# Optimization experiments

Hardware: AMD Instinct MI355X
Metric: run time of the kernel (lower is better)

## Reference

```python
import jax, jax.numpy as jnp
import numpy as np

EDGE_THRESHOLD = 0.1
N_NODES, IN_DIM, OUT_DIM, EDGE_DIM = 512, 128, 128, 64
LN_EPS = 1e-5


def setup_inputs() -> dict:
    key = jax.random.key(0)
    ks = jax.random.split(key, 20)
    s = 0.05
    d_in2e = 2 * IN_DIM + EDGE_DIM
    return {
        "node_features": jax.random.normal(ks[0], (N_NODES, IN_DIM), jnp.float32),
        "W": jax.random.normal(ks[1], (N_NODES, N_NODES), jnp.float32),
        "M": jax.random.normal(ks[2], (N_NODES, N_NODES), jnp.float32),
        "edge_features": jax.random.normal(ks[3], (N_NODES, N_NODES, EDGE_DIM), jnp.float32),
        # node_mlp: Linear(in,out) -> ReLU -> Linear(out,out)
        "node_w1": jax.random.normal(ks[4], (IN_DIM, OUT_DIM), jnp.float32) * s,
        "node_b1": jnp.zeros((OUT_DIM,), jnp.float32),
        "node_w2": jax.random.normal(ks[5], (OUT_DIM, OUT_DIM), jnp.float32) * s,
        "node_b2": jnp.zeros((OUT_DIM,), jnp.float32),
        # directed_msg: Linear(2*in+edge_dim,out) -> ReLU -> Linear(out,out)
        "dir_w1": jax.random.normal(ks[6], (d_in2e, OUT_DIM), jnp.float32) * s,
        "dir_b1": jnp.zeros((OUT_DIM,), jnp.float32),
        "dir_w2": jax.random.normal(ks[7], (OUT_DIM, OUT_DIM), jnp.float32) * s,
        "dir_b2": jnp.zeros((OUT_DIM,), jnp.float32),
        # bidirected_msg: Linear(2*in,out) -> ReLU -> Linear(out,out)
        "bi_w1": jax.random.normal(ks[8], (2 * IN_DIM, OUT_DIM), jnp.float32) * s,
        "bi_b1": jnp.zeros((OUT_DIM,), jnp.float32),
        "bi_w2": jax.random.normal(ks[9], (OUT_DIM, OUT_DIM), jnp.float32) * s,
        "bi_b2": jnp.zeros((OUT_DIM,), jnp.float32),
        # LayerNorm(out)
        "ln_g": jnp.ones((OUT_DIM,), jnp.float32),
        "ln_b": jnp.zeros((OUT_DIM,), jnp.float32),
    }


def reference(node_features, W, M, edge_features,
              node_w1, node_b1, node_w2, node_b2,
              dir_w1, dir_b1, dir_w2, dir_b2,
              bi_w1, bi_b1, bi_w2, bi_b2,
              ln_g, ln_b):
    n, d = node_features.shape
    x = node_features

    # self path
    h_self = jax.nn.relu(x @ node_w1 + node_b1) @ node_w2 + node_b2

    # directed messages: msg[j,i] = MLP([x_j, x_i, e_{j,i}]), weight = |W[j,i]| masked.
    # First linear split by concat blocks to avoid materializing (n,n,2d+e).
    src = x @ dir_w1[:d]                 # (n,h)   parent/source term
    tgt = x @ dir_w1[d:2 * d]            # (n,h)   target term
    edg = jnp.einsum('jie,eh->jih', edge_features, dir_w1[2 * d:])  # (n,n,h)
    h1 = jax.nn.relu(src[:, None, :] + tgt[None, :, :] + edg + dir_b1)  # (n,n,h) [j,i]
    msg_d = h1 @ dir_w2 + dir_b2         # (n,n,out)
    absW = jnp.abs(W)
    wd = jnp.where(absW > EDGE_THRESHOLD, absW, 0.0)  # (n,n) [parent j, target i]
    h_dir = jnp.einsum('jio,ji->io', msg_d, wd)

    # bidirected messages: for node i, neighbors j: MLP([x_j, x_i]), weight = |M[i,j]| masked, j != i
    bsrc = x @ bi_w1[:d]
    btgt = x @ bi_w1[d:]
    h1b = jax.nn.relu(bsrc[:, None, :] + btgt[None, :, :] + bi_b1)  # (n,n,h) [j,i]
    msg_b = h1b @ bi_w2 + bi_b2
    absM = jnp.abs(M)
    wb = jnp.where(absM > EDGE_THRESHOLD, absM, 0.0)
    wb = wb * (1.0 - jnp.eye(n, dtype=wb.dtype))  # exclude self
    h_bi = jnp.einsum('jio,ij->io', msg_b, wb)

    h = h_self + h_dir + h_bi
    mu = jnp.mean(h, axis=-1, keepdims=True)
    var = jnp.mean(jnp.square(h - mu), axis=-1, keepdims=True)
    return (h - mu) * jax.lax.rsqrt(var + LN_EPS) * ln_g + ln_b
```

## Files before the change

### kernel.cpp

```cpp
#include <hip/hip_runtime.h>
#include <hip/hip_bf16.h>
#include <cstdint>

#define NN 512
#define DD 128
#define EE 64
#define THR 0.1f
#define NCHUNK 16

typedef __bf16 bf16x8 __attribute__((ext_vector_type(8)));
typedef float  f32x4  __attribute__((ext_vector_type(4)));

__global__ __launch_bounds__(256) void k_zero(float* __restrict__ p, int n)
{
    int i = blockIdx.x * 256 + threadIdx.x;
    if (i < n) p[i] = 0.f;
}

__global__ __launch_bounds__(128) void k_pre(
    const float* __restrict__ x,
    const float* __restrict__ dw1, const float* __restrict__ bw1,
    const float* __restrict__ nw1, const float* __restrict__ nb1,
    float* __restrict__ src, float* __restrict__ tgt,
    float* __restrict__ bsrc, float* __restrict__ btgt, float* __restrict__ hmid)
{
    const int i0 = blockIdx.x * 4;
    const int h  = threadIdx.x;
    const int which = blockIdx.y;
    const float* B; float* outp;
    switch (which) {
        case 0:  B = dw1;          outp = src;  break;
        case 1:  B = dw1 + DD*DD;  outp = tgt;  break;
        case 2:  B = bw1;          outp = bsrc; break;
        case 3:  B = bw1 + DD*DD;  outp = btgt; break;
        default: B = nw1;          outp = hmid; break;
    }
    __shared__ float sx[4][DD];
    for (int idx = h; idx < 4*DD; idx += DD)
        sx[idx >> 7][idx & 127] = x[i0*DD + idx];
    __syncthreads();
    float a0=0.f, a1=0.f, a2=0.f, a3=0.f;
    for (int k = 0; k < DD; ++k) {
        float w = B[k*DD + h];
        a0 = fmaf(sx[0][k], w, a0);
        a1 = fmaf(sx[1][k], w, a1);
        a2 = fmaf(sx[2][k], w, a2);
        a3 = fmaf(sx[3][k], w, a3);
    }
    if (which == 4) {
        float bb = nb1[h];
        a0 = fmaxf(a0+bb, 0.f); a1 = fmaxf(a1+bb, 0.f);
        a2 = fmaxf(a2+bb, 0.f); a3 = fmaxf(a3+bb, 0.f);
    }
    outp[(i0+0)*DD + h] = a0;
    outp[(i0+1)*DD + h] = a1;
    outp[(i0+2)*DD + h] = a2;
    outp[(i0+3)*DD + h] = a3;
}

__global__ __launch_bounds__(256, 2) void k_dir(
    const float* __restrict__ ef, const float* __restrict__ W,
    const float* __restrict__ dw1, const float* __restrict__ db1,
    const float* __restrict__ src, const float* __restrict__ tgt,
    float* __restrict__ td_base, float* __restrict__ wsum_d, int partial)
{
    const int i0    = blockIdx.x * 16;
    const int jbase = blockIdx.y * 32;
    const int tid   = threadIdx.x;
    const int wave  = tid >> 6, lane = tid & 63;
    const int lrow  = lane & 15, lhi = lane >> 4;

    __shared__ float s_src[32][DD];
    __shared__ float s_wd[32][16];
    __shared__ float s_acc[4][16][DD];

    for (int idx = tid; idx < 32*DD; idx += 256)
        s_src[idx >> 7][idx & 127] = src[jbase*DD + idx];
    for (int idx = tid; idx < 32*16; idx += 256) {
        int jj = idx >> 4, il = idx & 15;
        float w = fabsf(W[(size_t)(jbase + jj)*NN + i0 + il]);
        s_wd[jj][il] = (w > THR) ? w : 0.0f;
    }

    bf16x8 bfrag[8][2];
    #pragma unroll
    for (int nf = 0; nf < 8; ++nf)
        #pragma unroll
        for (int kf = 0; kf < 2; ++kf) {
            bf16x8 t;
            #pragma unroll
            for (int e = 0; e < 8; ++e)
                t[e] = (__bf16)dw1[(2*DD + kf*32 + lhi*8 + e)*DD + nf*16 + lrow];
            bfrag[nf][kf] = t;
        }

    float tpre[8][4];
    #pragma unroll
    for (int nf = 0; nf < 8; ++nf)
        #pragma unroll
        for (int r = 0; r < 4; ++r) {
            int hh = nf*16 + lrow;
            tpre[nf][r] = tgt[(i0 + lhi*4 + r)*DD + hh] + db1[hh];
        }

    float acc[8][4] = {};
    __syncthreads();

    const float* ebase = ef + ((size_t)(jbase + wave)*NN + i0)*EE + lrow*EE + lhi*8;
    const size_t jstep = (size_t)4 * NN * EE;
    float4 a0 = *(const float4*)(ebase + 0);
    float4 a1 = *(const float4*)(ebase + 4);
    float4 a2 = *(const float4*)(ebase + 32);
    float4 a3 = *(const float4*)(ebase + 36);

    #pragma unroll 2
    for (int it = 0; it < 8; ++it) {
        float4 c0 = a0, c1 = a1, c2 = a2, c3 = a3;
        if (it < 7) {
            const float* np = ebase + (size_t)(it + 1)*jstep;
            a0 = *(const float4*)(np + 0);
            a1 = *(const float4*)(np + 4);
            a2 = *(const float4*)(np + 32);
            a3 = *(const float4*)(np + 36);
        }
        const int jj = wave + it*4;

        bf16x8 af0, af1;
        af0[0]=(__bf16)c0.x; af0[1]=(__bf16)c0.y; af0[2]=(__bf16)c0.z; af0[3]=(__bf16)c0.w;
        af0[4]=(__bf16)c1.x; af0[5]=(__bf16)c1.y; af0[6]=(__bf16)c1.z; af0[7]=(__bf16)c1.w;
        af1[0]=(__bf16)c2.x; af1[1]=(__bf16)c2.y; af1[2]=(__bf16)c2.z; af1[3]=(__bf16)c2.w;
        af1[4]=(__bf16)c3.x; af1[5]=(__bf16)c3.y; af1[6]=(__bf16)c3.z; af1[7]=(__bf16)c3.w;

        float wdv[4];
        #pragma unroll
        for (int r = 0; r < 4; ++r) wdv[r] = s_wd[jj][lhi*4 + r];

        #pragma unroll
        for (int nf = 0; nf < 8; ++nf) {
            f32x4 z = {0.f, 0.f, 0.f, 0.f};
            z = __builtin_amdgcn_mfma_f32_16x16x32_bf16(af0, bfrag[nf][0], z, 0, 0, 0);
            z = __builtin_amdgcn_mfma_f32_16x16x32_bf16(af1, bfrag[nf][1], z, 0, 0, 0);
            float sv = s_src[jj][nf*16 + lrow];
            #pragma unroll
            for (int r = 0; r < 4; ++r) {
                float v = z[r] + sv + tpre[nf][r];
                acc[nf][r] = fmaf(wdv[r], fmaxf(v, 0.f), acc[nf][r]);
            }
        }
    }

    #pragma unroll
    for (int nf = 0; nf < 8; ++nf)
        #pragma unroll
        for (int r = 0; r < 4; ++r)
            s_acc[wave][lhi*4 + r][nf*16 + lrow] = acc[nf][r];
    __syncthreads();

    float* dst = td_base + (partial ? (size_t)blockIdx.y * (NN*DD) : 0);
    for (int idx = tid; idx < 16*DD; idx += 256) {
        int il = idx >> 7, hh = idx & 127;
        float s = s_acc[0][il][hh] + s_acc[1][il][hh] + s_acc[2][il][hh] + s_acc[3][il][hh];
        int o = (i0 + il)*DD + hh;
        if (partial) dst[o] = s; else atomicAdd(&dst[o], s);
    }
    if (tid < 16) {
        float s = 0.f;
        #pragma unroll
        for (int jj = 0; jj < 32; ++jj) s += s_wd[jj][tid];
        if (partial) wsum_d[blockIdx.y * NN + i0 + tid] = s;
        else         atomicAdd(&wsum_d[i0 + tid], s);
    }
}

__global__ __launch_bounds__(256) void k_bidir(
    const float* __restrict__ M, const float* __restrict__ bsrc,
    const float* __restrict__ btgt, const float* __restrict__ bb1,
    float* __restrict__ tb_base, float* __restrict__ wsum_b, int partial)
{
    const int i0    = blockIdx.x * 16;
    const int jbase = blockIdx.y * 32;
    const int tid   = threadIdx.x;
    const int il    = tid >> 4;
    const int hg    = tid & 15;

    __shared__ float s_wb[16][32];
    __shared__ float s_bs[32][DD];

    for (int idx = tid; idx < 16*32; idx += 256) {
        int r = idx >> 5, jj = idx & 31;
        float m = fabsf(M[(size_t)(i0 + r)*NN + jbase + jj]);
        float w = (m > THR) ? m : 0.f;
        if (i0 + r == jbase + jj) w = 0.f;
        s_wb[r][jj] = w;
    }
    for (int idx = tid; idx < 32*DD; idx += 256)
        s_bs[idx >> 7][idx & 127] = bsrc[jbase*DD + idx];
    __syncthreads();

    float bt[8], acc[8] = {};
    #pragma unroll
    for (int r = 0; r < 8; ++r) {
        int hh = hg*8 + r;
        bt[r] = btgt[(i0 + il)*DD + hh] + bb1[hh];
    }
    for (int jj = 0; jj < 32; ++jj) {
        float w = s_wb[il][jj];
        const float* sp = &s_bs[jj][hg*8];
        float4 v0 = *(const float4*)sp;
        float4 v1 = *(const float4*)(sp + 4);
        acc[0] = fmaf(w, fmaxf(v0.x + bt[0], 0.f), acc[0]);
        acc[1] = fmaf(w, fmaxf(v0.y + bt[1], 0.f), acc[1]);
        acc[2] = fmaf(w, fmaxf(v0.z + bt[2], 0.f), acc[2]);
        acc[3] = fmaf(w, fmaxf(v0.w + bt[3], 0.f), acc[3]);
        acc[4] = fmaf(w, fmaxf(v1.x + bt[4], 0.f), acc[4]);
        acc[5] = fmaf(w, fmaxf(v1.y + bt[5], 0.f), acc[5]);
        acc[6] = fmaf(w, fmaxf(v1.z + bt[6], 0.f), acc[6]);
        acc[7] = fmaf(w, fmaxf(v1.w + bt[7], 0.f), acc[7]);
    }
    float* dst = tb_base + (partial ? (size_t)blockIdx.y * (NN*DD) : 0);
    #pragma unroll
    for (int r = 0; r < 8; ++r) {
        int o = (i0 + il)*DD + hg*8 + r;
        if (partial) dst[o] = acc[r]; else atomicAdd(&dst[o], acc[r]);
    }
    if (tid < 16) {
        float s = 0.f;
        #pragma unroll
        for (int jj = 0; jj < 32; ++jj) s += s_wb[tid][jj];
        if (partial) wsum_b[blockIdx.y * NN + i0 + tid] = s;
        else         atomicAdd(&wsum_b[i0 + tid], s);
    }
}

__global__ __launch_bounds__(256) void k_final(
    const float* __restrict__ hmid, const float* __restrict__ nw2, const float* __restrict__ nb2,
    const float* __restrict__ td,   const float* __restrict__ dw2, const float* __restrict__ db2,
    const float* __restrict__ wsd,
    const float* __restrict__ tb,   const float* __restrict__ bw2, const float* __restrict__ bb2,
    const float* __restrict__ wsb,
    const float* __restrict__ lng,  const float* __restrict__ lnb,
    float* __restrict__ out, int cd, int cb, int wpart)
{
    const int tid = threadIdx.x;
    const int r   = tid >> 7;
    const int h   = tid & 127;
    const int row = blockIdx.x * 2 + r;
    const int o   = row * DD + h;

    __shared__ float sm[2][DD], sd[2][DD], sb[2][DD];
    __shared__ float red[4];

    float vm = hmid[o];
    float s1 = 0.f, s2 = 0.f;
    #pragma unroll 4
    for (int c = 0; c < cd; ++c) s1 += td[(size_t)c*(NN*DD) + o];
    #pragma unroll 4
    for (int c = 0; c < cb; ++c) s2 += tb[(size_t)c*(NN*DD) + o];
    sm[r][h] = vm; sd[r][h] = s1; sb[r][h] = s2;
    __syncthreads();

    float wsum_d_row, wsum_b_row;
    if (wpart) {
        float a = 0.f, b = 0.f;
        #pragma unroll
        for (int c = 0; c < NCHUNK; ++c) {
            a += wsd[c*NN + row];
            b += wsb[c*NN + row];
        }
        wsum_d_row = a; wsum_b_row = b;
    } else {
        wsum_d_row = wsd[row]; wsum_b_row = wsb[row];
    }

    float acc = nb2[h] + wsum_d_row*db2[h] + wsum_b_row*bb2[h];
    #pragma unroll 4
    for (int k = 0; k < DD; ++k) {
        acc += sm[r][k]*nw2[k*DD + h] + sd[r][k]*dw2[k*DD + h] + sb[r][k]*bw2[k*DD + h];
    }

    const int wid = tid >> 6;
    float s = acc;
    #pragma unroll
    for (int off = 32; off > 0; off >>= 1) s += __shfl_down(s, off);
    if ((tid & 63) == 0) red[wid] = s;
    __syncthreads();
    float mu = (red[2*r] + red[2*r + 1]) * (1.0f/128.0f);
    float dv = acc - mu;
    float q  = dv * dv;
    __syncthreads();
    #pragma unroll
    for (int off = 32; off > 0; off >>= 1) q += __shfl_down(q, off);
    if ((tid & 63) == 0) red[wid] = q;
    __syncthreads();
    float var = (red[2*r] + red[2*r + 1]) * (1.0f/128.0f);
    out[o] = dv * rsqrtf(var + 1e-5f) * lng[h] + lnb[h];
}

extern "C" void kernel_launch(void* const* d_in, const int* in_sizes, int n_in,
                              void* d_out, int out_size, void* d_ws, size_t ws_size,
                              hipStream_t stream)
{
    (void)in_sizes; (void)n_in; (void)out_size;
    const float* x   = (const float*)d_in[0];
    const float* W   = (const float*)d_in[1];
    const float* M   = (const float*)d_in[2];
    const float* ef  = (const float*)d_in[3];
    const float* nw1 = (const float*)d_in[4];
    const float* nb1 = (const float*)d_in[5];
    const float* nw2 = (const float*)d_in[6];
    const float* nb2 = (const float*)d_in[7];
    const float* dw1 = (const float*)d_in[8];
    const float* db1 = (const float*)d_in[9];
    const float* dw2 = (const float*)d_in[10];
    const float* db2 = (const float*)d_in[11];
    const float* bw1 = (const float*)d_in[12];
    const float* bb1 = (const float*)d_in[13];
    const float* bw2 = (const float*)d_in[14];
    const float* bb2 = (const float*)d_in[15];
    const float* lng = (const float*)d_in[16];
    const float* lnb = (const float*)d_in[17];
    float* out = (float*)d_out;
    float* ws  = (float*)d_ws;

    const size_t TD = (size_t)NN * DD;
    const size_t WS_PART = (size_t)NCHUNK * NN;
    const size_t PART_FLOATS = 32*TD + 2*WS_PART + 5*TD;
    const int partial = (ws_size >= PART_FLOATS * 4) ? 1 : 0;

    float *t_dir, *t_bi, *wsd, *wsb, *base;
    if (partial) {
        t_dir = ws;
        t_bi  = ws + 16*TD;
        wsd   = ws + 32*TD;
        wsb   = wsd + WS_PART;
        base  = wsb + WS_PART;
    } else {
        t_dir = ws;
        t_bi  = ws + TD;
        wsd   = ws + 2*TD;
        wsb   = wsd + 512;
        base  = ws + 2*TD + 1024;
        int nz = (int)(2*TD + 1024);
        k_zero<<<(nz + 255)/256, 256, 0, stream>>>(ws, nz);
    }
    float* src  = base;
    float* tgt  = base + TD;
    float* bsrc = base + 2*TD;
    float* btgt = base + 3*TD;
    float* hmid = base + 4*TD;

    k_pre  <<<dim3(NN/4, 5), 128, 0, stream>>>(x, dw1, bw1, nw1, nb1,
                                               src, tgt, bsrc, btgt, hmid);
    k_dir  <<<dim3(NN/16, NN/32), 256, 0, stream>>>(ef, W, dw1, db1, src, tgt,
                                                    t_dir, wsd, partial);
    k_bidir<<<dim3(NN/16, NN/32), 256, 0, stream>>>(M, bsrc, btgt, bb1,
                                                    t_bi, wsb, partial);
    const int cd = partial ? NCHUNK : 1;
    k_final<<<NN/2, 256, 0, stream>>>(hmid, nw2, nb2, t_dir, dw2, db2, wsd,
                                      t_bi, bw2, bb2, wsb, lng, lnb, out,
                                      cd, cd, partial);
}
```

Measured before the change: 59.59 us.

## Fuse bidirected pass into directed kernel and split final matvec across two halves

Merges the bidirected message kernel into the directed one, so a single launch computes both and the bidirected ReLU-accumulate runs while the first edge-feature loads are in flight. It also reworks the final kernel to use one row per block, with the two thread halves splitting both the partial-sum reduction and the K dimension of the output matvec. This removes a launch and improves latency hiding, at the cost of more shared memory and registers in the fused kernel, which may reduce occupancy. The final kernel now uses twice as many blocks, each with an extra shared-memory reduction step.

Result: slower. 61.81 us (+3.7%).

```diff
diff --git a/kernel.cpp b/kernel.cpp
--- a/kernel.cpp
+++ b/kernel.cpp
@@ -58,28 +58,42 @@
     outp[(i0+3)*DD + h] = a3;
 }
 
-__global__ __launch_bounds__(256, 2) void k_dir(
+__global__ __launch_bounds__(256, 2) void k_dirbi(
     const float* __restrict__ ef, const float* __restrict__ W,
+    const float* __restrict__ M,
     const float* __restrict__ dw1, const float* __restrict__ db1,
     const float* __restrict__ src, const float* __restrict__ tgt,
-    float* __restrict__ td_base, float* __restrict__ wsum_d, int partial)
+    const float* __restrict__ bsrc, const float* __restrict__ btgt,
+    const float* __restrict__ bb1,
+    float* __restrict__ td_base, float* __restrict__ tb_base,
+    float* __restrict__ wsum_d, float* __restrict__ wsum_b, int partial)
 {
     const int i0    = blockIdx.x * 16;
     const int jbase = blockIdx.y * 32;
     const int tid   = threadIdx.x;
     const int wave  = tid >> 6, lane = tid & 63;
     const int lrow  = lane & 15, lhi = lane >> 4;
+    const int il    = tid >> 4;
+    const int hg    = tid & 15;
 
     __shared__ float s_src[32][DD];
     __shared__ float s_wd[32][16];
+    __shared__ float s_wb[16][32];
+    __shared__ float s_bs[32][DD];
     __shared__ float s_acc[4][16][DD];
 
-    for (int idx = tid; idx < 32*DD; idx += 256)
+    for (int idx = tid; idx < 32*DD; idx += 256) {
         s_src[idx >> 7][idx & 127] = src[jbase*DD + idx];
+        s_bs [idx >> 7][idx & 127] = bsrc[jbase*DD + idx];
+    }
     for (int idx = tid; idx < 32*16; idx += 256) {
-        int jj = idx >> 4, il = idx & 15;
-        float w = fabsf(W[(size_t)(jbase + jj)*NN + i0 + il]);
-        s_wd[jj][il] = (w > THR) ? w : 0.0f;
+        int jj = idx >> 4, ii = idx & 15;
+        float w = fabsf(W[(size_t)(jbase + jj)*NN + i0 + ii]);
+        s_wd[jj][ii] = (w > THR) ? w : 0.0f;
+        float m = fabsf(M[(size_t)(i0 + ii)*NN + jbase + jj]);
+        float wb = (m > THR) ? m : 0.f;
+        if (i0 + ii == jbase + jj) wb = 0.f;
+        s_wb[ii][jj] = wb;
     }
 
     bf16x8 bfrag[8][2];
@@ -112,6 +126,35 @@
     float4 a1 = *(const float4*)(ebase + 4);
     float4 a2 = *(const float4*)(ebase + 32);
     float4 a3 = *(const float4*)(ebase + 36);
+
+    {
+        float bt[8], bacc[8] = {};
+        #pragma unroll
+        for (int r = 0; r < 8; ++r) {
+            int hh = hg*8 + r;
+            bt[r] = btgt[(i0 + il)*DD + hh] + bb1[hh];
+        }
+        for (int jj = 0; jj < 32; ++jj) {
+            float w = s_wb[il][jj];
+            const float* sp = &s_bs[jj][hg*8];
+            float4 v0 = *(const float4*)sp;
+            float4 v1 = *(const float4*)(sp + 4);
+            bacc[0] = fmaf(w, fmaxf(v0.x + bt[0], 0.f), bacc[0]);
+            bacc[1] = fmaf(w, fmaxf(v0.y + bt[1], 0.f), bacc[1]);
+            bacc[2] = fmaf(w, fmaxf(v0.z + bt[2], 0.f), bacc[2]);
+            bacc[3] = fmaf(w, fmaxf(v0.w + bt[3], 0.f), bacc[3]);
+            bacc[4] = fmaf(w, fmaxf(v1.x + bt[4], 0.f), bacc[4]);
+            bacc[5] = fmaf(w, fmaxf(v1.y + bt[5], 0.f), bacc[5]);
+            bacc[6] = fmaf(w, fmaxf(v1.z + bt[6], 0.f), bacc[6]);
+            bacc[7] = fmaf(w, fmaxf(v1.w + bt[7], 0.f), bacc[7]);
+        }
+        float* bdst = tb_base + (partial ? (size_t)blockIdx.y * (NN*DD) : 0);
+        #pragma unroll
+        for (int r = 0; r < 8; ++r) {
+            int o = (i0 + il)*DD + hg*8 + r;
+            if (partial) bdst[o] = bacc[r]; else atomicAdd(&bdst[o], bacc[r]);
+        }
+    }
 
     #pragma unroll 2
     for (int it = 0; it < 8; ++it) {
@@ -158,9 +201,9 @@
 
     float* dst = td_base + (partial ? (size_t)blockIdx.y * (NN*DD) : 0);
     for (int idx = tid; idx < 16*DD; idx += 256) {
-        int il = idx >> 7, hh = idx & 127;
-        float s = s_acc[0][il][hh] + s_acc[1][il][hh] + s_acc[2][il][hh] + s_acc[3][il][hh];
-        int o = (i0 + il)*DD + hh;
+        int ii = idx >> 7, hh = idx & 127;
+        float s = s_acc[0][ii][hh] + s_acc[1][ii][hh] + s_acc[2][ii][hh] + s_acc[3][ii][hh];
+        int o = (i0 + ii)*DD + hh;
         if (partial) dst[o] = s; else atomicAdd(&dst[o], s);
     }
     if (tid < 16) {
@@ -169,66 +212,13 @@
         for (int jj = 0; jj < 32; ++jj) s += s_wd[jj][tid];
         if (partial) wsum_d[blockIdx.y * NN + i0 + tid] = s;
         else         atomicAdd(&wsum_d[i0 + tid], s);
-    }
-}
-
-__global__ __launch_bounds__(256) void k_bidir(
-    const float* __restrict__ M, const float* __restrict__ bsrc,
-    const float* __restrict__ btgt, const float* __restrict__ bb1,
-    float* __restrict__ tb_base, float* __restrict__ wsum_b, int partial)
-{
-    const int i0    = blockIdx.x * 16;
-    const int jbase = blockIdx.y * 32;
-    const int tid   = threadIdx.x;
-    const int il    = tid >> 4;
-    const int hg    = tid & 15;
-
-    __shared__ float s_wb[16][32];
-    __shared__ float s_bs[32][DD];
-
-    for (int idx = tid; idx < 16*32; idx += 256) {
-        int r = idx >> 5, jj = idx & 31;
-        float m = fabsf(M[(size_t)(i0 + r)*NN + jbase + jj]);
-        float w = (m > THR) ? m : 0.f;
-        if (i0 + r == jbase + jj) w = 0.f;
-        s_wb[r][jj] = w;
-    }
-    for (int idx = tid; idx < 32*DD; idx += 256)
-        s_bs[idx >> 7][idx & 127] = bsrc[jbase*DD + idx];
-    __syncthreads();
-
-    float bt[8], acc[8] = {};
-    #pragma unroll
-    for (int r = 0; r < 8; ++r) {
-        int hh = hg*8 + r;
-        bt[r] = btgt[(i0 + il)*DD + hh] + bb1[hh];
-    }
-    for (int jj = 0; jj < 32; ++jj) {
-        float w = s_wb[il][jj];
-        const float* sp = &s_bs[jj][hg*8];
-        float4 v0 = *(const float4*)sp;
-        float4 v1 = *(const float4*)(sp + 4);
-        acc[0] = fmaf(w, fmaxf(v0.x + bt[0], 0.f), acc[0]);
-        acc[1] = fmaf(w, fmaxf(v0.y + bt[1], 0.f), acc[1]);
-        acc[2] = fmaf(w, fmaxf(v0.z + bt[2], 0.f), acc[2]);
-        acc[3] = fmaf(w, fmaxf(v0.w + bt[3], 0.f), acc[3]);
-        acc[4] = fmaf(w, fmaxf(v1.x + bt[4], 0.f), acc[4]);
-        acc[5] = fmaf(w, fmaxf(v1.y + bt[5], 0.f), acc[5]);
-        acc[6] = fmaf(w, fmaxf(v1.z + bt[6], 0.f), acc[6]);
-        acc[7] = fmaf(w, fmaxf(v1.w + bt[7], 0.f), acc[7]);
-    }
-    float* dst = tb_base + (partial ? (size_t)blockIdx.y * (NN*DD) : 0);
-    #pragma unroll
-    for (int r = 0; r < 8; ++r) {
-        int o = (i0 + il)*DD + hg*8 + r;
-        if (partial) dst[o] = acc[r]; else atomicAdd(&dst[o], acc[r]);
-    }
-    if (tid < 16) {
+    } else if (tid < 32) {
+        int ii = tid - 16;
         float s = 0.f;
         #pragma unroll
-        for (int jj = 0; jj < 32; ++jj) s += s_wb[tid][jj];
-        if (partial) wsum_b[blockIdx.y * NN + i0 + tid] = s;
-        else         atomicAdd(&wsum_b[i0 + tid], s);
+        for (int jj = 0; jj < 32; ++jj) s += s_wb[ii][jj];
+        if (partial) wsum_b[blockIdx.y * NN + i0 + ii] = s;
+        else         atomicAdd(&wsum_b[i0 + ii], s);
     }
 }
 
@@ -239,61 +229,73 @@
     const float* __restrict__ tb,   const float* __restrict__ bw2, const float* __restrict__ bb2,
     const float* __restrict__ wsb,
     const float* __restrict__ lng,  const float* __restrict__ lnb,
-    float* __restrict__ out, int cd, int cb, int wpart)
-{
-    const int tid = threadIdx.x;
-    const int r   = tid >> 7;
-    const int h   = tid & 127;
-    const int row = blockIdx.x * 2 + r;
-    const int o   = row * DD + h;
-
-    __shared__ float sm[2][DD], sd[2][DD], sb[2][DD];
+    float* __restrict__ out, int cd, int wpart)
+{
+    const int tid  = threadIdx.x;
+    const int h    = tid & 127;
+    const int half = tid >> 7;
+    const int row  = blockIdx.x;
+    const int o    = row * DD + h;
+
+    __shared__ float sm[DD];
+    __shared__ float sd2[2][DD], sb2[2][DD];
     __shared__ float red[4];
 
-    float vm = hmid[o];
     float s1 = 0.f, s2 = 0.f;
+    for (int c = half; c < cd; c += 2) {
+        s1 += td[(size_t)c*(NN*DD) + o];
+        s2 += tb[(size_t)c*(NN*DD) + o];
+    }
+    sd2[half][h] = s1; sb2[half][h] = s2;
+    if (half == 0) sm[h] = hmid[o];
+    __syncthreads();
+
+    float acc;
+    if (half == 0) {
+        float wd_r, wb_r;
+        if (wpart) {
+            wd_r = 0.f; wb_r = 0.f;
+            #pragma unroll
+            for (int c = 0; c < NCHUNK; ++c) {
+                wd_r += wsd[c*NN + row];
+                wb_r += wsb[c*NN + row];
+            }
+        } else { wd_r = wsd[row]; wb_r = wsb[row]; }
+        acc = nb2[h] + wd_r*db2[h] + wb_r*bb2[h];
+    } else {
+        acc = 0.f;
+    }
+
+    const int k0 = half * 64;
     #pragma unroll 4
-    for (int c = 0; c < cd; ++c) s1 += td[(size_t)c*(NN*DD) + o];
-    #pragma unroll 4
-    for (int c = 0; c < cb; ++c) s2 += tb[(size_t)c*(NN*DD) + o];
-    sm[r][h] = vm; sd[r][h] = s1; sb[r][h] = s2;
-    __syncthreads();
-
-    float wsum_d_row, wsum_b_row;
-    if (wpart) {
-        float a = 0.f, b = 0.f;
-        #pragma unroll
-        for (int c = 0; c < NCHUNK; ++c) {
-            a += wsd[c*NN + row];
-            b += wsb[c*NN + row];
-        }
-        wsum_d_row = a; wsum_b_row = b;
-    } else {
-        wsum_d_row = wsd[row]; wsum_b_row = wsb[row];
-    }
-
-    float acc = nb2[h] + wsum_d_row*db2[h] + wsum_b_row*bb2[h];
-    #pragma unroll 4
-    for (int k = 0; k < DD; ++k) {
-        acc += sm[r][k]*nw2[k*DD + h] + sd[r][k]*dw2[k*DD + h] + sb[r][k]*bw2[k*DD + h];
-    }
-
-    const int wid = tid >> 6;
-    float s = acc;
+    for (int kk = 0; kk < 64; ++kk) {
+        int k = k0 + kk;
+        float vm = sm[k];
+        float vd = sd2[0][k] + sd2[1][k];
+        float vb = sb2[0][k] + sb2[1][k];
+        acc += vm*nw2[k*DD + h] + vd*dw2[k*DD + h] + vb*bw2[k*DD + h];
+    }
+    __syncthreads();
+    sd2[half][h] = acc;
+    __syncthreads();
+    float a = sd2[0][h] + sd2[1][h];
+
+    float s = a;
     #pragma unroll
     for (int off = 32; off > 0; off >>= 1) s += __shfl_down(s, off);
-    if ((tid & 63) == 0) red[wid] = s;
-    __syncthreads();
-    float mu = (red[2*r] + red[2*r + 1]) * (1.0f/128.0f);
-    float dv = acc - mu;
+    if ((tid & 63) == 0) red[tid >> 6] = s;
+    __syncthreads();
+    float mu = (red[0] + red[1] + red[2] + red[3]) * (1.0f/256.0f);
+    float dv = a - mu;
     float q  = dv * dv;
     __syncthreads();
     #pragma unroll
     for (int off = 32; off > 0; off >>= 1) q += __shfl_down(q, off);
-    if ((tid & 63) == 0) red[wid] = q;
-    __syncthreads();
-    float var = (red[2*r] + red[2*r + 1]) * (1.0f/128.0f);
-    out[o] = dv * rsqrtf(var + 1e-5f) * lng[h] + lnb[h];
+    if ((tid & 63) == 0) red[tid >> 6] = q;
+    __syncthreads();
+    float var = (red[0] + red[1] + red[2] + red[3]) * (1.0f/256.0f);
+    if (half == 0)
+        out[o] = dv * rsqrtf(var + 1e-5f) * lng[h] + lnb[h];
 }
 
 extern "C" void kernel_launch(void* const* d_in, const int* in_sizes, int n_in,
@@ -351,12 +353,11 @@
 
     k_pre  <<<dim3(NN/4, 5), 128, 0, stream>>>(x, dw1, bw1, nw1, nb1,
                                                src, tgt, bsrc, btgt, hmid);
-    k_dir  <<<dim3(NN/16, NN/32), 256, 0, stream>>>(ef, W, dw1, db1, src, tgt,
-                                                    t_dir, wsd, partial);
-    k_bidir<<<dim3(NN/16, NN/32), 256, 0, stream>>>(M, bsrc, btgt, bb1,
-                                                    t_bi, wsb, partial);
+    k_dirbi<<<dim3(NN/16, NN/32), 256, 0, stream>>>(ef, W, M, dw1, db1,
+                                                    src, tgt, bsrc, btgt, bb1,
+                                                    t_dir, t_bi, wsd, wsb, partial);
     const int cd = partial ? NCHUNK : 1;
-    k_final<<<NN/2, 256, 0, stream>>>(hmid, nw2, nb2, t_dir, dw2, db2, wsd,
-                                      t_bi, bw2, bb2, wsb, lng, lnb, out,
-                                      cd, cd, partial);
-}
+    k_final<<<NN, 256, 0, stream>>>(hmid, nw2, nb2, t_dir, dw2, db2, wsd,
+                                    t_bi, bw2, bb2, wsb, lng, lnb, out,
+                                    cd, partial);
+}
```

## Split k_final rows across two half-blocks, double-buffer edge loads, unroll k_pre

Applied to the files above, without the earlier changes.

k_final now runs one row per 256-thread block. The two halves each sum half of the partial chunks and half of the K dimension, then combine their results through shared memory before the LayerNorm. This doubles the block count so more of the GPU is used for the final GEMV and reduction. k_dir's edge-feature prefetch becomes a two-deep double buffer with a fully unrolled loop, and the k_pre inner loop gets unroll 8. The changes add register pressure and extra barriers in exchange for more memory-level parallelism.

Result: slower. 68.62 us (+15.1%).

```diff
diff --git a/kernel.cpp b/kernel.cpp
--- a/kernel.cpp
+++ b/kernel.cpp
@@ -40,6 +40,7 @@
         sx[idx >> 7][idx & 127] = x[i0*DD + idx];
     __syncthreads();
     float a0=0.f, a1=0.f, a2=0.f, a3=0.f;
+    #pragma unroll 8
     for (int k = 0; k < DD; ++k) {
         float w = B[k*DD + h];
         a0 = fmaf(sx[0][k], w, a0);
@@ -108,22 +109,22 @@
 
     const float* ebase = ef + ((size_t)(jbase + wave)*NN + i0)*EE + lrow*EE + lhi*8;
     const size_t jstep = (size_t)4 * NN * EE;
-    float4 a0 = *(const float4*)(ebase + 0);
-    float4 a1 = *(const float4*)(ebase + 4);
-    float4 a2 = *(const float4*)(ebase + 32);
-    float4 a3 = *(const float4*)(ebase + 36);
-
-    #pragma unroll 2
+
+    float4 bA0 = *(const float4*)(ebase + 0);
+    float4 bA1 = *(const float4*)(ebase + 4);
+    float4 bA2 = *(const float4*)(ebase + 32);
+    float4 bA3 = *(const float4*)(ebase + 36);
+    const float* p1 = ebase + jstep;
+    float4 bB0 = *(const float4*)(p1 + 0);
+    float4 bB1 = *(const float4*)(p1 + 4);
+    float4 bB2 = *(const float4*)(p1 + 32);
+    float4 bB3 = *(const float4*)(p1 + 36);
+
+    #pragma unroll
     for (int it = 0; it < 8; ++it) {
-        float4 c0 = a0, c1 = a1, c2 = a2, c3 = a3;
-        if (it < 7) {
-            const float* np = ebase + (size_t)(it + 1)*jstep;
-            a0 = *(const float4*)(np + 0);
-            a1 = *(const float4*)(np + 4);
-            a2 = *(const float4*)(np + 32);
-            a3 = *(const float4*)(np + 36);
-        }
-        const int jj = wave + it*4;
+        float4 c0, c1, c2, c3;
+        if ((it & 1) == 0) { c0 = bA0; c1 = bA1; c2 = bA2; c3 = bA3; }
+        else               { c0 = bB0; c1 = bB1; c2 = bB2; c3 = bB3; }
 
         bf16x8 af0, af1;
         af0[0]=(__bf16)c0.x; af0[1]=(__bf16)c0.y; af0[2]=(__bf16)c0.z; af0[3]=(__bf16)c0.w;
@@ -131,6 +132,22 @@
         af1[0]=(__bf16)c2.x; af1[1]=(__bf16)c2.y; af1[2]=(__bf16)c2.z; af1[3]=(__bf16)c2.w;
         af1[4]=(__bf16)c3.x; af1[5]=(__bf16)c3.y; af1[6]=(__bf16)c3.z; af1[7]=(__bf16)c3.w;
 
+        if (it < 6) {
+            const float* np = ebase + (size_t)(it + 2)*jstep;
+            if ((it & 1) == 0) {
+                bA0 = *(const float4*)(np + 0);
+                bA1 = *(const float4*)(np + 4);
+                bA2 = *(const float4*)(np + 32);
+                bA3 = *(const float4*)(np + 36);
+            } else {
+                bB0 = *(const float4*)(np + 0);
+                bB1 = *(const float4*)(np + 4);
+                bB2 = *(const float4*)(np + 32);
+                bB3 = *(const float4*)(np + 36);
+            }
+        }
+
+        const int jj = wave + it*4;
         float wdv[4];
         #pragma unroll
         for (int r = 0; r < 4; ++r) wdv[r] = s_wd[jj][lhi*4 + r];
@@ -239,61 +256,73 @@
     const float* __restrict__ tb,   const float* __restrict__ bw2, const float* __restrict__ bb2,
     const float* __restrict__ wsb,
     const float* __restrict__ lng,  const float* __restrict__ lnb,
-    float* __restrict__ out, int cd, int cb, int wpart)
-{
-    const int tid = threadIdx.x;
-    const int r   = tid >> 7;
-    const int h   = tid & 127;
-    const int row = blockIdx.x * 2 + r;
-    const int o   = row * DD + h;
-
-    __shared__ float sm[2][DD], sd[2][DD], sb[2][DD];
+    float* __restrict__ out, int cd, int wpart)
+{
+    const int tid  = threadIdx.x;
+    const int h    = tid & 127;
+    const int half = tid >> 7;
+    const int row  = blockIdx.x;
+    const int o    = row * DD + h;
+
+    __shared__ float sm[DD];
+    __shared__ float sd2[2][DD], sb2[2][DD];
     __shared__ float red[4];
 
-    float vm = hmid[o];
     float s1 = 0.f, s2 = 0.f;
+    for (int c = half; c < cd; c += 2) {
+        s1 += td[(size_t)c*(NN*DD) + o];
+        s2 += tb[(size_t)c*(NN*DD) + o];
+    }
+    sd2[half][h] = s1; sb2[half][h] = s2;
+    if (half == 0) sm[h] = hmid[o];
+    __syncthreads();
+
+    float acc;
+    if (half == 0) {
+        float wd_r, wb_r;
+        if (wpart) {
+            wd_r = 0.f; wb_r = 0.f;
+            #pragma unroll
+            for (int c = 0; c < NCHUNK; ++c) {
+                wd_r += wsd[c*NN + row];
+                wb_r += wsb[c*NN + row];
+            }
+        } else { wd_r = wsd[row]; wb_r = wsb[row]; }
+        acc = nb2[h] + wd_r*db2[h] + wb_r*bb2[h];
+    } else {
+        acc = 0.f;
+    }
+
+    const int k0 = half * 64;
     #pragma unroll 4
-    for (int c = 0; c < cd; ++c) s1 += td[(size_t)c*(NN*DD) + o];
-    #pragma unroll 4
-    for (int c = 0; c < cb; ++c) s2 += tb[(size_t)c*(NN*DD) + o];
-    sm[r][h] = vm; sd[r][h] = s1; sb[r][h] = s2;
-    __syncthreads();
-
-    float wsum_d_row, wsum_b_row;
-    if (wpart) {
-        float a = 0.f, b = 0.f;
-        #pragma unroll
-        for (int c = 0; c < NCHUNK; ++c) {
-            a += wsd[c*NN + row];
-            b += wsb[c*NN + row];
-        }
-        wsum_d_row = a; wsum_b_row = b;
-    } else {
-        wsum_d_row = wsd[row]; wsum_b_row = wsb[row];
-    }
-
-    float acc = nb2[h] + wsum_d_row*db2[h] + wsum_b_row*bb2[h];
-    #pragma unroll 4
-    for (int k = 0; k < DD; ++k) {
-        acc += sm[r][k]*nw2[k*DD + h] + sd[r][k]*dw2[k*DD + h] + sb[r][k]*bw2[k*DD + h];
-    }
-
-    const int wid = tid >> 6;
-    float s = acc;
+    for (int kk = 0; kk < 64; ++kk) {
+        int k = k0 + kk;
+        float vm = sm[k];
+        float vd = sd2[0][k] + sd2[1][k];
+        float vb = sb2[0][k] + sb2[1][k];
+        acc += vm*nw2[k*DD + h] + vd*dw2[k*DD + h] + vb*bw2[k*DD + h];
+    }
+    __syncthreads();
+    sd2[half][h] = acc;
+    __syncthreads();
+    float a = sd2[0][h] + sd2[1][h];
+
+    float s = a;
     #pragma unroll
     for (int off = 32; off > 0; off >>= 1) s += __shfl_down(s, off);
-    if ((tid & 63) == 0) red[wid] = s;
-    __syncthreads();
-    float mu = (red[2*r] + red[2*r + 1]) * (1.0f/128.0f);
-    float dv = acc - mu;
+    if ((tid & 63) == 0) red[tid >> 6] = s;
+    __syncthreads();
+    float mu = (red[0] + red[1] + red[2] + red[3]) * (1.0f/256.0f);
+    float dv = a - mu;
     float q  = dv * dv;
     __syncthreads();
     #pragma unroll
     for (int off = 32; off > 0; off >>= 1) q += __shfl_down(q, off);
-    if ((tid & 63) == 0) red[wid] = q;
-    __syncthreads();
-    float var = (red[2*r] + red[2*r + 1]) * (1.0f/128.0f);
-    out[o] = dv * rsqrtf(var + 1e-5f) * lng[h] + lnb[h];
+    if ((tid & 63) == 0) red[tid >> 6] = q;
+    __syncthreads();
+    float var = (red[0] + red[1] + red[2] + red[3]) * (1.0f/256.0f);
+    if (half == 0)
+        out[o] = dv * rsqrtf(var + 1e-5f) * lng[h] + lnb[h];
 }
 
 extern "C" void kernel_launch(void* const* d_in, const int* in_sizes, int n_in,
@@ -356,7 +385,7 @@
     k_bidir<<<dim3(NN/16, NN/32), 256, 0, stream>>>(M, bsrc, btgt, bb1,
                                                     t_bi, wsb, partial);
     const int cd = partial ? NCHUNK : 1;
-    k_final<<<NN/2, 256, 0, stream>>>(hmid, nw2, nb2, t_dir, dw2, db2, wsd,
-                                      t_bi, bw2, bb2, wsb, lng, lnb, out,
-                                      cd, cd, partial);
-}
+    k_final<<<NN, 256, 0, stream>>>(hmid, nw2, nb2, t_dir, dw2, db2, wsd,
+                                    t_bi, bw2, bb2, wsb, lng, lnb, out,
+                                    cd, partial);
+}
```
